# Kernel tuning notes

Measured on AMD Instinct MI355X. Metric: run time of the kernel, lower is better.

## Reference

```python
import jax, jax.numpy as jnp
import numpy as np

N, CIN, HID, COUT = 10000, 128, 64, 40
EPS = 1e-5  # torch BatchNorm1d default

def _bn(x, g, b):
    # training-mode batch norm, biased variance (torch normalization convention)
    mu = x.mean(0)
    var = x.var(0)
    return g * (x - mu) * jax.lax.rsqrt(var + EPS) + b

def _spectral(X, La, U, va, vb):
    # out_A2 @ out_A @ X with out_A = U diag(La^va) U^T, out_A2 = U diag(((2(La-1e-8)-1)^2+1)^vb) U^T
    # O(N^2 d) factored form instead of materializing N x N matrices via diag().
    v1 = jnp.power(La, va)
    v2 = jnp.power((2.0 * (La - 1e-8) - 1.0) ** 2 + 1.0, vb)
    t = v1[:, None] * (U.T @ X)   # [N, d]
    t = U @ t                     # out_A @ X
    t = v2[:, None] * (U.T @ t)
    return U @ t                  # out_A2 @ out_A @ X

def setup_inputs():
    key = jax.random.key(0)
    ks = jax.random.split(key, 16)
    d = {}
    d['X'] = jax.random.normal(ks[0], (N, CIN), jnp.float32)
    d['La'] = jax.random.uniform(ks[1], (N,), jnp.float32, minval=0.05, maxval=1.0)
    d['U'] = jax.random.normal(ks[2], (N, N), jnp.float32) / np.float32(np.sqrt(N))

    def lin(k, i, o):
        k1, k2 = jax.random.split(k)
        return (jax.random.normal(k1, (i, o), jnp.float32) / np.float32(np.sqrt(i)),
                jax.random.normal(k2, (o,), jnp.float32) * 0.01)

    dims_in = [CIN, HID, HID]
    lin_out = [HID, HID, COUT]
    idx = 3
    for i in range(3):
        d[f'va{i}'] = jnp.asarray(7.0, jnp.float32)  # Velocity(7)
        d[f'vb{i}'] = jnp.asarray(0.0, jnp.float32)  # Velocity(0)
        w, b = lin(ks[idx], dims_in[i], HID); idx += 1
        d[f'Wb{i}_w'], d[f'Wb{i}_b'] = w, b          # SLOG_B.W
        d[f'bn1g{i}'] = jnp.ones((HID,), jnp.float32)
        d[f'bn1b{i}'] = jnp.zeros((HID,), jnp.float32)
        w, b = lin(ks[idx], dims_in[i], lin_out[i]); idx += 1
        d[f'lin{i}_w'], d[f'lin{i}_b'] = w, b        # self.lines[i]
        if i < 2:
            d[f'bn2g{i}'] = jnp.ones((HID,), jnp.float32)
            d[f'bn2b{i}'] = jnp.zeros((HID,), jnp.float32)
    w, b = lin(ks[idx], HID, COUT)
    d['mlp_w'], d['mlp_b'] = w, b                    # SLOG_N.MLP
    return d

def reference(X, La, U,
              va0, vb0, Wb0_w, Wb0_b, bn1g0, bn1b0, lin0_w, lin0_b, bn2g0, bn2b0,
              va1, vb1, Wb1_w, Wb1_b, bn1g1, bn1b1, lin1_w, lin1_b, bn2g1, bn2b1,
              va2, vb2, Wb2_w, Wb2_b, bn1g2, bn1b2, lin2_w, lin2_b,
              mlp_w, mlp_b):
    def block(Xi, va, vb, Ww, Wbias, g1, b1, lw, lb, g2, b2):
        h = _spectral(Xi, La, U, va, vb) @ Ww + Wbias     # hidden_emd from SLOG_B
        h = jax.nn.relu(_bn(h, g1, b1))                   # bns1[i] + ReLU (dropout=eval id)
        Xn = jax.nn.relu(h + Xi @ lw + lb)                # residual lines[i]
        return _bn(Xn, g2, b2)                            # bns2[i]
    X = block(X, va0, vb0, Wb0_w, Wb0_b, bn1g0, bn1b0, lin0_w, lin0_b, bn2g0, bn2b0)
    X = block(X, va1, vb1, Wb1_w, Wb1_b, bn1g1, bn1b1, lin1_w, lin1_b, bn2g1, bn2b1)
    h = _spectral(X, La, U, va2, vb2) @ Wb2_w + Wb2_b
    h = jax.nn.relu(_bn(h, bn1g2, bn1b2))
    out = jax.nn.sigmoid(h @ mlp_w + mlp_b) + X @ lin2_w + lin2_b
    return jax.nn.log_softmax(out, axis=1)
```

## Files before the change

kernel.cpp:

```cpp
#include <hip/hip_runtime.h>
#include <math.h>

#define NP 10000
#define KPAD 10048
#define KS 8
#define KC 1280
#define EPSBN 1e-5f

typedef _Float16 h8 __attribute__((ext_vector_type(8)));
typedef float f4 __attribute__((ext_vector_type(4)));

__device__ __forceinline__ void gload_lds16(const _Float16* g, _Float16* l) {
    __builtin_amdgcn_global_load_lds(
        (const __attribute__((address_space(1))) unsigned int*)g,
        (__attribute__((address_space(3))) unsigned int*)l,
        16, 0, 0);
}


__global__ __launch_bounds__(256) void compute_v_kern(
    const float* __restrict__ La, const float* __restrict__ vap,
    const float* __restrict__ vbp, float* __restrict__ v1, float* __restrict__ v2)
{
    int i = blockIdx.x * 256 + threadIdx.x;
    if (i >= NP) return;
    float la = La[i];
    float va = vap[0], vb = vbp[0];
    v1[i] = powf(la, va);
    float w = 2.0f * (la - 1e-8f) - 1.0f;
    v2[i] = powf(w * w + 1.0f, vb);
}

__global__ __launch_bounds__(256) void reduce_partials(
    const float* __restrict__ P, float* __restrict__ out, int nz, int count)
{
    const int i = (blockIdx.x * 256 + threadIdx.x) * 4;
    if (i >= count) return;
    float4 a = *(const float4*)(P + i);
    for (int z = 1; z < nz; ++z) {
        float4 b = *(const float4*)(P + (size_t)z * count + i);
        a.x += b.x; a.y += b.y; a.z += b.z; a.w += b.w;
    }
    *(float4*)(out + i) = a;
}

__global__ __launch_bounds__(256) void dual_linear_kern(
    const float* __restrict__ S, const float* __restrict__ Xin,
    const float* __restrict__ Ww, const float* __restrict__ wb,
    const float* __restrict__ Lw, const float* __restrict__ lb,
    float* __restrict__ h, float* __restrict__ r,
    double* __restrict__ sum1, double* __restrict__ sq1,
    int din, int dl)
{
    __shared__ float Sr[4][128];
    __shared__ float Xr[4][128];
    __shared__ float hsh[4][64];
    const int tid = threadIdx.x;
    const int row0 = blockIdx.x * 4;
    for (int idx = tid; idx < 4 * din; idx += 256) {
        const int rr = idx / din;
        const int k  = idx - rr * din;
        Sr[rr][k] = S  [(size_t)(row0 + rr) * din + k];
        Xr[rr][k] = Xin[(size_t)(row0 + rr) * din + k];
    }
    __syncthreads();
    const int rr = tid >> 6;
    const int c  = tid & 63;
    float acc = wb[c];
    for (int k = 0; k < din; ++k) acc = fmaf(Sr[rr][k], Ww[k * 64 + c], acc);
    h[(size_t)(row0 + rr) * 64 + c] = acc;
    hsh[rr][c] = acc;
    if (c < dl) {
        float a2 = lb[c];
        for (int k = 0; k < din; ++k) a2 = fmaf(Xr[rr][k], Lw[k * dl + c], a2);
        r[(size_t)(row0 + rr) * dl + c] = a2;
    }
    __syncthreads();
    if (tid < 64) {
        float s = hsh[0][tid] + hsh[1][tid] + hsh[2][tid] + hsh[3][tid];
        float q = hsh[0][tid] * hsh[0][tid] + hsh[1][tid] * hsh[1][tid]
                + hsh[2][tid] * hsh[2][tid] + hsh[3][tid] * hsh[3][tid];
        atomicAdd(&sum1[tid], (double)s);
        atomicAdd(&sq1[tid],  (double)q);
    }
}

__global__ void bn_finalize_kern(const double* __restrict__ sum, const double* __restrict__ sq,
                                 float* __restrict__ mean, float* __restrict__ rstd)
{
    const int c = threadIdx.x;
    double m   = sum[c] / (double)NP;
    double var = sq[c] / (double)NP - m * m;
    mean[c] = (float)m;
    rstd[c] = rsqrtf((float)var + EPSBN);
}

__global__ __launch_bounds__(256) void apply1_kern(
    const float* __restrict__ h, const float* __restrict__ r,
    const float* __restrict__ g1, const float* __restrict__ b1,
    const float* __restrict__ mean1, const float* __restrict__ rstd1,
    float* __restrict__ Xn, double* __restrict__ sum2, double* __restrict__ sq2)
{
    __shared__ float sh[256];
    __shared__ float sh2[256];
    const int tid = threadIdx.x;
    const int idx = blockIdx.x * 256 + tid;
    const int c = tid & 63;
    float v = h[idx];
    v = fmaf(g1[c] * (v - mean1[c]), rstd1[c], b1[c]);
    v = fmaxf(v, 0.f);
    float x = fmaxf(v + r[idx], 0.f);
    Xn[idx] = x;
    sh[tid]  = x;
    sh2[tid] = x * x;
    __syncthreads();
    if (tid < 64) {
        float s = sh[tid]  + sh[tid + 64]  + sh[tid + 128]  + sh[tid + 192];
        float q = sh2[tid] + sh2[tid + 64] + sh2[tid + 128] + sh2[tid + 192];
        atomicAdd(&sum2[tid], (double)s);
        atomicAdd(&sq2[tid],  (double)q);
    }
}

__global__ __launch_bounds__(256) void apply2_kern(
    const float* __restrict__ Xn, const float* __restrict__ g2, const float* __restrict__ b2,
    const float* __restrict__ mean2, const float* __restrict__ rstd2, float* __restrict__ Xout)
{
    const int idx = blockIdx.x * 256 + threadIdx.x;
    const int c = idx & 63;
    Xout[idx] = fmaf(g2[c] * (Xn[idx] - mean2[c]), rstd2[c], b2[c]);
}

__global__ __launch_bounds__(64) void final_row_kern(
    const float* __restrict__ h, const float* __restrict__ r40,
    const float* __restrict__ g1, const float* __restrict__ b1,
    const float* __restrict__ mean1, const float* __restrict__ rstd1,
    const float* __restrict__ mlp_w, const float* __restrict__ mlp_b,
    float* __restrict__ out)
{
    __shared__ float hh[64];
    __shared__ float o[40];
    __shared__ float lse;
    const int row = blockIdx.x;
    const int j = threadIdx.x;
    float v = h[(size_t)row * 64 + j];
    v = fmaf(g1[j] * (v - mean1[j]), rstd1[j], b1[j]);
    hh[j] = fmaxf(v, 0.f);
    __syncthreads();
    if (j < 40) {
        float acc = mlp_b[j];
        #pragma unroll
        for (int c2 = 0; c2 < 64; ++c2) acc = fmaf(hh[c2], mlp_w[c2 * 40 + j], acc);
        float s = 1.0f / (1.0f + expf(-acc));
        o[j] = s + r40[(size_t)row * 40 + j];
    }
    __syncthreads();
    if (j == 0) {
        float m = -1e30f;
        for (int t = 0; t < 40; ++t) m = fmaxf(m, o[t]);
        float se = 0.f;
        for (int t = 0; t < 40; ++t) se += expf(o[t] - m);
        lse = m + logf(se);
    }
    __syncthreads();
    if (j < 40) out[(size_t)row * 40 + j] = o[j] - lse;
}


__global__ __launch_bounds__(256) void convert_u_kern(
    const float* __restrict__ U, _Float16* __restrict__ U16, _Float16* __restrict__ U16T)
{
    __shared__ float S[64][68];
    const int tid = threadIdx.x;
    const int r0 = blockIdx.x * 64, c0 = blockIdx.y * 64;
    const int r  = tid >> 2;
    const int cq = (tid & 3) * 16;
    const int gr = r0 + r;
    float v[16];
    const bool cvalid = (c0 + cq + 16 <= NP);
    if (gr < NP && cvalid) {
        const float* src = U + (size_t)gr * NP + c0 + cq;
        float4 a = *(const float4*)(src);
        float4 b = *(const float4*)(src + 4);
        float4 c = *(const float4*)(src + 8);
        float4 d = *(const float4*)(src + 12);
        v[0]=a.x; v[1]=a.y; v[2]=a.z; v[3]=a.w; v[4]=b.x; v[5]=b.y; v[6]=b.z; v[7]=b.w;
        v[8]=c.x; v[9]=c.y; v[10]=c.z; v[11]=c.w; v[12]=d.x; v[13]=d.y; v[14]=d.z; v[15]=d.w;
    } else {
        #pragma unroll
        for (int j = 0; j < 16; ++j) v[j] = 0.f;
    }
    if (gr < NP) {
        h8 x0, x1;
        #pragma unroll
        for (int j = 0; j < 8; ++j) { x0[j] = (_Float16)v[j]; x1[j] = (_Float16)v[8 + j]; }
        _Float16* dst = U16 + (size_t)gr * KPAD + c0 + cq;
        *(h8*)(dst) = x0;
        *(h8*)(dst + 8) = x1;
    }
    #pragma unroll
    for (int j = 0; j < 16; ++j) S[r][cq + j] = v[j];
    __syncthreads();
    const int oc = c0 + (tid >> 2);
    const int kq = (tid & 3) * 16;
    if (oc < NP) {
        h8 x0, x1;
        #pragma unroll
        for (int j = 0; j < 8; ++j) {
            x0[j] = (_Float16)S[kq + j][tid >> 2];
            x1[j] = (_Float16)S[kq + 8 + j][tid >> 2];
        }
        _Float16* dst = U16T + (size_t)oc * KPAD + r0 + kq;
        *(h8*)(dst) = x0;
        *(h8*)(dst + 8) = x1;
    }
}

__global__ __launch_bounds__(256) void bt_kern(
    const float* __restrict__ src, const float* __restrict__ vs,
    _Float16* __restrict__ Bt, int d)
{
    __shared__ float S[64][68];
    const int tid = threadIdx.x;
    const int k0 = blockIdx.x * 64, n0 = blockIdx.y * 64;
    const int r  = tid >> 2;
    const int cq = (tid & 3) * 16;
    const int gk = k0 + r;
    float v[16];
    if (gk < NP) {
        const float sc = vs ? vs[gk] : 1.0f;
        const float* sp = src + (size_t)gk * d + n0 + cq;
        float4 a = *(const float4*)(sp);
        float4 b = *(const float4*)(sp + 4);
        float4 c = *(const float4*)(sp + 8);
        float4 e = *(const float4*)(sp + 12);
        v[0]=a.x*sc; v[1]=a.y*sc; v[2]=a.z*sc; v[3]=a.w*sc;
        v[4]=b.x*sc; v[5]=b.y*sc; v[6]=b.z*sc; v[7]=b.w*sc;
        v[8]=c.x*sc; v[9]=c.y*sc; v[10]=c.z*sc; v[11]=c.w*sc;
        v[12]=e.x*sc; v[13]=e.y*sc; v[14]=e.z*sc; v[15]=e.w*sc;
    } else {
        #pragma unroll
        for (int j = 0; j < 16; ++j) v[j] = 0.f;
    }
    #pragma unroll
    for (int j = 0; j < 16; ++j) S[r][cq + j] = v[j];
    __syncthreads();
    const int on = n0 + (tid >> 2);
    const int kq = (tid & 3) * 16;
    h8 x0, x1;
    #pragma unroll
    for (int j = 0; j < 8; ++j) {
        x0[j] = (_Float16)S[kq + j][tid >> 2];
        x1[j] = (_Float16)S[kq + 8 + j][tid >> 2];
    }
    _Float16* dst = Bt + (size_t)on * KPAD + k0 + kq;
    *(h8*)(dst) = x0;
    *(h8*)(dst + 8) = x1;
}

__global__ __launch_bounds__(256) void reduce_to_bt(
    const float* __restrict__ P, const float* __restrict__ vs,
    _Float16* __restrict__ Bt, int cnt, int dshift)
{
    const int e4 = (blockIdx.x * 256 + threadIdx.x) * 4;
    if (e4 >= cnt) return;
    float4 a = *(const float4*)(P + e4);
    #pragma unroll
    for (int z = 1; z < KS; ++z) {
        float4 b = *(const float4*)(P + (size_t)z * cnt + e4);
        a.x += b.x; a.y += b.y; a.z += b.z; a.w += b.w;
    }
    const int k = e4 >> dshift;
    const int n = e4 & ((1 << dshift) - 1);
    const float s = vs ? vs[k] : 1.0f;
    Bt[(size_t)(n + 0) * KPAD + k] = (_Float16)(a.x * s);
    Bt[(size_t)(n + 1) * KPAD + k] = (_Float16)(a.y * s);
    Bt[(size_t)(n + 2) * KPAD + k] = (_Float16)(a.z * s);
    Bt[(size_t)(n + 3) * KPAD + k] = (_Float16)(a.w * s);
}

template<int R>
__device__ __forceinline__ void stage_rows(
    const _Float16* __restrict__ g, _Float16* lds, size_t row0, int k0,
    int wave, int lane)
{
    const int rsub = lane >> 3;
    const int csub = lane & 7;
    const int c    = csub ^ rsub;
    #pragma unroll
    for (int j = wave; j < R / 8; j += 4) {
        const size_t grow = row0 + (size_t)(j * 8 + rsub);
        gload_lds16(g + grow * KPAD + k0 + c * 8, lds + j * 512);
    }
}

template<int BN>
__global__ __launch_bounds__(256) void mfma_gemm(
    const _Float16* __restrict__ A, const _Float16* __restrict__ Bt,
    float* __restrict__ P)
{
    constexpr int WN  = BN / 2;
    constexpr int WTN = BN / 32;
    __shared__ _Float16 As[128 * 64];
    __shared__ _Float16 Bs[BN * 64];

    const int tid  = threadIdx.x;
    const int m0   = blockIdx.x * 128;
    const int z    = blockIdx.z;
    const int k_begin = z * KC;
    const int k_end   = min(KPAD, k_begin + KC);
    const int lane = tid & 63;
    const int wave = tid >> 6;
    const int wm = wave & 1, wn = wave >> 1;
    const int lr = lane & 15, quad = lane >> 4;

    f4 acc[4][WTN];
    #pragma unroll
    for (int i = 0; i < 4; ++i)
        #pragma unroll
        for (int j = 0; j < WTN; ++j) {
            f4 zz = {0.f, 0.f, 0.f, 0.f};
            acc[i][j] = zz;
        }

    for (int k0 = k_begin; k0 < k_end; k0 += 64) {
        stage_rows<128>(A, As, (size_t)m0, k0, wave, lane);
        stage_rows<BN>(Bt, Bs, 0, k0, wave, lane);
        __syncthreads();
        #pragma unroll
        for (int g = 0; g < 2; ++g) {
            h8 af[4];
            h8 bf[WTN];
            #pragma unroll
            for (int i = 0; i < 4; ++i) {
                const int row = wm * 64 + i * 16 + lr;
                af[i] = *(const h8*)(As + row * 64 + ((((g << 2) | quad) ^ (row & 7)) << 3));
            }
            #pragma unroll
            for (int j = 0; j < WTN; ++j) {
                const int row = wn * WN + j * 16 + lr;
                bf[j] = *(const h8*)(Bs + row * 64 + ((((g << 2) | quad) ^ (row & 7)) << 3));
            }
            #pragma unroll
            for (int i = 0; i < 4; ++i)
                #pragma unroll
                for (int j = 0; j < WTN; ++j)
                    acc[i][j] = __builtin_amdgcn_mfma_f32_16x16x32_f16(af[i], bf[j], acc[i][j], 0, 0, 0);
        }
        __syncthreads();
    }

    float* __restrict__ Cp = P + (size_t)z * (size_t)NP * (size_t)BN;
    #pragma unroll
    for (int i = 0; i < 4; ++i) {
        const int mb = m0 + wm * 64 + i * 16 + quad * 4;
        #pragma unroll
        for (int j = 0; j < WTN; ++j) {
            const int n = wn * WN + j * 16 + lr;
            #pragma unroll
            for (int r = 0; r < 4; ++r) {
                const int m = mb + r;
                if (m < NP) Cp[(size_t)m * BN + n] = acc[i][j][r];
            }
        }
    }
}


extern "C" void kernel_launch(void* const* d_in, const int* in_sizes, int n_in,
                              void* d_out, int out_size, void* d_ws, size_t ws_size,
                              hipStream_t stream)
{
    const float* X     = (const float*)d_in[0];
    const float* La    = (const float*)d_in[1];
    const float* U     = (const float*)d_in[2];
    const float* mlp_w = (const float*)d_in[31];
    const float* mlp_b = (const float*)d_in[32];

    char* ws = (char*)d_ws;
    size_t off = 0;
    auto alloc = [&](size_t bytes) -> void* {
        void* p = ws + off;
        off = (off + bytes + 255) & ~(size_t)255;
        return p;
    };

    _Float16* U16  = (_Float16*)alloc((size_t)10112 * KPAD * 2);
    _Float16* U16T = (_Float16*)alloc((size_t)10112 * KPAD * 2);
    _Float16* Bt   = (_Float16*)alloc((size_t)128 * KPAD * 2);
    float*  P     = (float*)alloc((size_t)KS * NP * 128 * 4);
    float*  bufB  = (float*)alloc((size_t)NP * 128 * 4);
    float*  h     = (float*)alloc((size_t)NP * 64 * 4);
    float*  r     = (float*)alloc((size_t)NP * 64 * 4);
    float*  Xn    = (float*)alloc((size_t)NP * 64 * 4);
    float*  Xbuf  = (float*)alloc((size_t)NP * 64 * 4);
    float*  v1    = (float*)alloc((size_t)NP * 4);
    float*  v2    = (float*)alloc((size_t)NP * 4);
    double* stats = (double*)alloc((size_t)3 * 256 * 8);
    float*  mr    = (float*)alloc((size_t)3 * 256 * 4);

    hipMemsetAsync(stats, 0, 3 * 256 * 8, stream);

    convert_u_kern<<<dim3(157, 157), 256, 0, stream>>>(U, U16, U16T);

    const float* Xcur = X;
    int din = 128;
    for (int i = 0; i < 3; ++i) {
        const int base = 3 + i * 10;
        const float* vap = (const float*)d_in[base + 0];
        const float* vbp = (const float*)d_in[base + 1];
        const float* Ww  = (const float*)d_in[base + 2];
        const float* wb  = (const float*)d_in[base + 3];
        const float* g1  = (const float*)d_in[base + 4];
        const float* b1  = (const float*)d_in[base + 5];
        const float* Lw  = (const float*)d_in[base + 6];
        const float* lb  = (const float*)d_in[base + 7];

        compute_v_kern<<<(NP + 255) / 256, 256, 0, stream>>>(La, vap, vbp, v1, v2);

        const int cnt    = NP * din;
        const int dshift = (din == 128) ? 7 : 6;
        const int rb     = cnt / 1024;
        dim3 gg(79, 1, KS);

        bt_kern<<<dim3(157, din / 64), 256, 0, stream>>>(Xcur, nullptr, Bt, din);
        if (din == 128) {
            mfma_gemm<128><<<gg, 256, 0, stream>>>(U16T, Bt, P);
            reduce_to_bt<<<rb, 256, 0, stream>>>(P, v1, Bt, cnt, dshift);
            mfma_gemm<128><<<gg, 256, 0, stream>>>(U16, Bt, P);
            reduce_to_bt<<<rb, 256, 0, stream>>>(P, nullptr, Bt, cnt, dshift);
            mfma_gemm<128><<<gg, 256, 0, stream>>>(U16T, Bt, P);
            reduce_to_bt<<<rb, 256, 0, stream>>>(P, v2, Bt, cnt, dshift);
            mfma_gemm<128><<<gg, 256, 0, stream>>>(U16, Bt, P);
            reduce_partials<<<rb, 256, 0, stream>>>(P, bufB, KS, cnt);
        } else {
            mfma_gemm<64><<<gg, 256, 0, stream>>>(U16T, Bt, P);
            reduce_to_bt<<<rb, 256, 0, stream>>>(P, v1, Bt, cnt, dshift);
            mfma_gemm<64><<<gg, 256, 0, stream>>>(U16, Bt, P);
            reduce_to_bt<<<rb, 256, 0, stream>>>(P, nullptr, Bt, cnt, dshift);
            mfma_gemm<64><<<gg, 256, 0, stream>>>(U16T, Bt, P);
            reduce_to_bt<<<rb, 256, 0, stream>>>(P, v2, Bt, cnt, dshift);
            mfma_gemm<64><<<gg, 256, 0, stream>>>(U16, Bt, P);
            reduce_partials<<<rb, 256, 0, stream>>>(P, bufB, KS, cnt);
        }

        const int dl = (i < 2) ? 64 : 40;
        double* sum1 = stats + i * 256;
        double* sq1  = sum1 + 64;
        double* sum2 = sum1 + 128;
        double* sq2  = sum1 + 192;
        float* mean1 = mr + i * 256;
        float* rstd1 = mean1 + 64;
        float* mean2 = mean1 + 128;
        float* rstd2 = mean1 + 192;

        dual_linear_kern<<<NP / 4, 256, 0, stream>>>(bufB, Xcur, Ww, wb, Lw, lb,
                                                     h, r, sum1, sq1, din, dl);
        bn_finalize_kern<<<1, 64, 0, stream>>>(sum1, sq1, mean1, rstd1);
        if (i < 2) {
            const float* g2 = (const float*)d_in[base + 8];
            const float* b2 = (const float*)d_in[base + 9];
            apply1_kern<<<NP / 4, 256, 0, stream>>>(h, r, g1, b1, mean1, rstd1, Xn, sum2, sq2);
            bn_finalize_kern<<<1, 64, 0, stream>>>(sum2, sq2, mean2, rstd2);
            apply2_kern<<<NP / 4, 256, 0, stream>>>(Xn, g2, b2, mean2, rstd2, Xbuf);
            Xcur = Xbuf;
            din = 64;
        } else {
            final_row_kern<<<NP, 64, 0, stream>>>(h, r, g1, b1, mean1, rstd1,
                                                  mlp_w, mlp_b, (float*)d_out);
        }
    }
}
```

Before: 1.761 ms.

## Shrink GEMM M-tile, raise split-K count, store fp16 partial sums

The split-K MFMA GEMM drops from 128-row to 64-row M tiles and from 8 to 10 K splits, taking the grid from 79x8 to 157x10 blocks. This fills more CUs for this skinny N x N by N x d product, which is bound by streaming U. Partial sums are now written and read as fp16 instead of fp32, halving partial traffic in the reduce kernels. In exchange, B tiles are reloaded from global memory more often per unit of A, there are more partials to reduce, and rounding each partial to fp16 loses some accuracy.

```diff
diff --git a/kernel.cpp b/kernel.cpp
--- a/kernel.cpp
+++ b/kernel.cpp
@@ -3,11 +3,12 @@
 
 #define NP 10000
 #define KPAD 10048
-#define KS 8
-#define KC 1280
+#define KS 10
+#define KC 1024
 #define EPSBN 1e-5f
 
 typedef _Float16 h8 __attribute__((ext_vector_type(8)));
+typedef _Float16 h4 __attribute__((ext_vector_type(4)));
 typedef float f4 __attribute__((ext_vector_type(4)));
 
 __device__ __forceinline__ void gload_lds16(const _Float16* g, _Float16* l) {
@@ -29,19 +30,6 @@
     v1[i] = powf(la, va);
     float w = 2.0f * (la - 1e-8f) - 1.0f;
     v2[i] = powf(w * w + 1.0f, vb);
-}
-
-__global__ __launch_bounds__(256) void reduce_partials(
-    const float* __restrict__ P, float* __restrict__ out, int nz, int count)
-{
-    const int i = (blockIdx.x * 256 + threadIdx.x) * 4;
-    if (i >= count) return;
-    float4 a = *(const float4*)(P + i);
-    for (int z = 1; z < nz; ++z) {
-        float4 b = *(const float4*)(P + (size_t)z * count + i);
-        a.x += b.x; a.y += b.y; a.z += b.z; a.w += b.w;
-    }
-    *(float4*)(out + i) = a;
 }
 
 __global__ __launch_bounds__(256) void dual_linear_kern(
@@ -259,24 +247,41 @@
 }
 
 __global__ __launch_bounds__(256) void reduce_to_bt(
-    const float* __restrict__ P, const float* __restrict__ vs,
+    const _Float16* __restrict__ P, const float* __restrict__ vs,
     _Float16* __restrict__ Bt, int cnt, int dshift)
 {
     const int e4 = (blockIdx.x * 256 + threadIdx.x) * 4;
     if (e4 >= cnt) return;
-    float4 a = *(const float4*)(P + e4);
+    h4 p = *(const h4*)(P + e4);
+    float a0 = (float)p[0], a1 = (float)p[1], a2 = (float)p[2], a3 = (float)p[3];
     #pragma unroll
     for (int z = 1; z < KS; ++z) {
-        float4 b = *(const float4*)(P + (size_t)z * cnt + e4);
-        a.x += b.x; a.y += b.y; a.z += b.z; a.w += b.w;
+        h4 q = *(const h4*)(P + (size_t)z * cnt + e4);
+        a0 += (float)q[0]; a1 += (float)q[1]; a2 += (float)q[2]; a3 += (float)q[3];
     }
     const int k = e4 >> dshift;
     const int n = e4 & ((1 << dshift) - 1);
     const float s = vs ? vs[k] : 1.0f;
-    Bt[(size_t)(n + 0) * KPAD + k] = (_Float16)(a.x * s);
-    Bt[(size_t)(n + 1) * KPAD + k] = (_Float16)(a.y * s);
-    Bt[(size_t)(n + 2) * KPAD + k] = (_Float16)(a.z * s);
-    Bt[(size_t)(n + 3) * KPAD + k] = (_Float16)(a.w * s);
+    Bt[(size_t)(n + 0) * KPAD + k] = (_Float16)(a0 * s);
+    Bt[(size_t)(n + 1) * KPAD + k] = (_Float16)(a1 * s);
+    Bt[(size_t)(n + 2) * KPAD + k] = (_Float16)(a2 * s);
+    Bt[(size_t)(n + 3) * KPAD + k] = (_Float16)(a3 * s);
+}
+
+__global__ __launch_bounds__(256) void reduce_partials(
+    const _Float16* __restrict__ P, float* __restrict__ out, int cnt)
+{
+    const int e4 = (blockIdx.x * 256 + threadIdx.x) * 4;
+    if (e4 >= cnt) return;
+    h4 p = *(const h4*)(P + e4);
+    float a0 = (float)p[0], a1 = (float)p[1], a2 = (float)p[2], a3 = (float)p[3];
+    #pragma unroll
+    for (int z = 1; z < KS; ++z) {
+        h4 q = *(const h4*)(P + (size_t)z * cnt + e4);
+        a0 += (float)q[0]; a1 += (float)q[1]; a2 += (float)q[2]; a3 += (float)q[3];
+    }
+    float4 o = make_float4(a0, a1, a2, a3);
+    *(float4*)(out + e4) = o;
 }
 
 template<int R>
@@ -297,15 +302,15 @@
 template<int BN>
 __global__ __launch_bounds__(256) void mfma_gemm(
     const _Float16* __restrict__ A, const _Float16* __restrict__ Bt,
-    float* __restrict__ P)
+    _Float16* __restrict__ P)
 {
     constexpr int WN  = BN / 2;
     constexpr int WTN = BN / 32;
-    __shared__ _Float16 As[128 * 64];
+    __shared__ _Float16 As[64 * 64];
     __shared__ _Float16 Bs[BN * 64];
 
     const int tid  = threadIdx.x;
-    const int m0   = blockIdx.x * 128;
+    const int m0   = blockIdx.x * 64;
     const int z    = blockIdx.z;
     const int k_begin = z * KC;
     const int k_end   = min(KPAD, k_begin + KC);
@@ -314,9 +319,9 @@
     const int wm = wave & 1, wn = wave >> 1;
     const int lr = lane & 15, quad = lane >> 4;
 
-    f4 acc[4][WTN];
-    #pragma unroll
-    for (int i = 0; i < 4; ++i)
+    f4 acc[2][WTN];
+    #pragma unroll
+    for (int i = 0; i < 2; ++i)
         #pragma unroll
         for (int j = 0; j < WTN; ++j) {
             f4 zz = {0.f, 0.f, 0.f, 0.f};
@@ -324,16 +329,16 @@
         }
 
     for (int k0 = k_begin; k0 < k_end; k0 += 64) {
-        stage_rows<128>(A, As, (size_t)m0, k0, wave, lane);
+        stage_rows<64>(A, As, (size_t)m0, k0, wave, lane);
         stage_rows<BN>(Bt, Bs, 0, k0, wave, lane);
         __syncthreads();
         #pragma unroll
         for (int g = 0; g < 2; ++g) {
-            h8 af[4];
+            h8 af[2];
             h8 bf[WTN];
             #pragma unroll
-            for (int i = 0; i < 4; ++i) {
-                const int row = wm * 64 + i * 16 + lr;
+            for (int i = 0; i < 2; ++i) {
+                const int row = wm * 32 + i * 16 + lr;
                 af[i] = *(const h8*)(As + row * 64 + ((((g << 2) | quad) ^ (row & 7)) << 3));
             }
             #pragma unroll
@@ -342,7 +347,7 @@
                 bf[j] = *(const h8*)(Bs + row * 64 + ((((g << 2) | quad) ^ (row & 7)) << 3));
             }
             #pragma unroll
-            for (int i = 0; i < 4; ++i)
+            for (int i = 0; i < 2; ++i)
                 #pragma unroll
                 for (int j = 0; j < WTN; ++j)
                     acc[i][j] = __builtin_amdgcn_mfma_f32_16x16x32_f16(af[i], bf[j], acc[i][j], 0, 0, 0);
@@ -350,17 +355,17 @@
         __syncthreads();
     }
 
-    float* __restrict__ Cp = P + (size_t)z * (size_t)NP * (size_t)BN;
-    #pragma unroll
-    for (int i = 0; i < 4; ++i) {
-        const int mb = m0 + wm * 64 + i * 16 + quad * 4;
+    _Float16* __restrict__ Cp = P + (size_t)z * (size_t)NP * (size_t)BN;
+    #pragma unroll
+    for (int i = 0; i < 2; ++i) {
+        const int mb = m0 + wm * 32 + i * 16 + quad * 4;
         #pragma unroll
         for (int j = 0; j < WTN; ++j) {
             const int n = wn * WN + j * 16 + lr;
             #pragma unroll
             for (int r = 0; r < 4; ++r) {
                 const int m = mb + r;
-                if (m < NP) Cp[(size_t)m * BN + n] = acc[i][j][r];
+                if (m < NP) Cp[(size_t)m * BN + n] = (_Float16)acc[i][j][r];
             }
         }
     }
@@ -388,7 +393,7 @@
     _Float16* U16  = (_Float16*)alloc((size_t)10112 * KPAD * 2);
     _Float16* U16T = (_Float16*)alloc((size_t)10112 * KPAD * 2);
     _Float16* Bt   = (_Float16*)alloc((size_t)128 * KPAD * 2);
-    float*  P     = (float*)alloc((size_t)KS * NP * 128 * 4);
+    _Float16* P    = (_Float16*)alloc((size_t)KS * NP * 128 * 2);
     float*  bufB  = (float*)alloc((size_t)NP * 128 * 4);
     float*  h     = (float*)alloc((size_t)NP * 64 * 4);
     float*  r     = (float*)alloc((size_t)NP * 64 * 4);
@@ -421,7 +426,7 @@
         const int cnt    = NP * din;
         const int dshift = (din == 128) ? 7 : 6;
         const int rb     = cnt / 1024;
-        dim3 gg(79, 1, KS);
+        dim3 gg(157, 1, KS);
 
         bt_kern<<<dim3(157, din / 64), 256, 0, stream>>>(Xcur, nullptr, Bt, din);
         if (din == 128) {
@@ -432,7 +437,7 @@
             mfma_gemm<128><<<gg, 256, 0, stream>>>(U16T, Bt, P);
             reduce_to_bt<<<rb, 256, 0, stream>>>(P, v2, Bt, cnt, dshift);
             mfma_gemm<128><<<gg, 256, 0, stream>>>(U16, Bt, P);
-            reduce_partials<<<rb, 256, 0, stream>>>(P, bufB, KS, cnt);
+            reduce_partials<<<rb, 256, 0, stream>>>(P, bufB, cnt);
         } else {
             mfma_gemm<64><<<gg, 256, 0, stream>>>(U16T, Bt, P);
             reduce_to_bt<<<rb, 256, 0, stream>>>(P, v1, Bt, cnt, dshift);
@@ -441,7 +446,7 @@
             mfma_gemm<64><<<gg, 256, 0, stream>>>(U16T, Bt, P);
             reduce_to_bt<<<rb, 256, 0, stream>>>(P, v2, Bt, cnt, dshift);
             mfma_gemm<64><<<gg, 256, 0, stream>>>(U16, Bt, P);
-            reduce_partials<<<rb, 256, 0, stream>>>(P, bufB, KS, cnt);
+            reduce_partials<<<rb, 256, 0, stream>>>(P, bufB, cnt);
         }
 
         const int dl = (i < 2) ? 64 : 40;
```

After: 1.768 ms. About the same (+0.4%).
